# Kernel tuning notes

Hardware: AMD Instinct MI355X
Metric: run time of the kernel (lower is better)

Reference implementation:

```python
import jax, jax.numpy as jnp
import numpy as np

B, S, D = 8, 4096, 256
NUM_WINDOW = 8
WIN = S // NUM_WINDOW          # 512
H = 2                          # num_heads
K = D                          # key_dim = d_model per source
DFF = 1024
LN_EPS = 1e-3                  # keras LayerNormalization default epsilon


def _layer_norm(x, g, b):
    mu = jnp.mean(x, axis=-1, keepdims=True)
    var = jnp.mean(jnp.square(x - mu), axis=-1, keepdims=True)
    return (x - mu) * jax.lax.rsqrt(var + LN_EPS) * g + b


def setup_inputs() -> dict:
    key = jax.random.key(0)
    ks = jax.random.split(key, 12)
    s = 0.02
    inp = {
        "x": jax.random.normal(ks[0], (B, S, D), dtype=jnp.float32),
        # MHA projections (keras MultiHeadAttention layout)
        "Wq": jax.random.normal(ks[1], (D, H, K), dtype=jnp.float32) * s,
        "bq": jnp.zeros((H, K), dtype=jnp.float32),
        "Wk": jax.random.normal(ks[2], (D, H, K), dtype=jnp.float32) * s,
        "bk": jnp.zeros((H, K), dtype=jnp.float32),
        "Wv": jax.random.normal(ks[3], (D, H, K), dtype=jnp.float32) * s,
        "bv": jnp.zeros((H, K), dtype=jnp.float32),
        "Wo": jax.random.normal(ks[4], (H, K, D), dtype=jnp.float32) * s,
        "bo": jnp.zeros((D,), dtype=jnp.float32),
        "ln1_g": jnp.ones((D,), dtype=jnp.float32),
        "ln1_b": jnp.zeros((D,), dtype=jnp.float32),
        # FeedForward
        "W1": jax.random.normal(ks[5], (D, DFF), dtype=jnp.float32) * s,
        "b1": jnp.zeros((DFF,), dtype=jnp.float32),
        "W2": jax.random.normal(ks[6], (DFF, D), dtype=jnp.float32) * s,
        "b2": jnp.zeros((D,), dtype=jnp.float32),
        "ln2_g": jnp.ones((D,), dtype=jnp.float32),
        "ln2_b": jnp.zeros((D,), dtype=jnp.float32),
    }
    return inp


def reference(x, Wq, bq, Wk, bk, Wv, bv, Wo, bo, ln1_g, ln1_b,
              W1, b1, W2, b2, ln2_g, ln2_b):
    # --- Localized self-attention: block-diagonal over NUM_WINDOW windows ---
    xw = x.reshape(B, NUM_WINDOW, WIN, D)               # [b, w, s, d]
    q = jnp.einsum('bwsd,dhk->bwshk', xw, Wq) + bq      # [b, w, s, h, k]
    k = jnp.einsum('bwsd,dhk->bwshk', xw, Wk) + bk
    v = jnp.einsum('bwsd,dhk->bwshk', xw, Wv) + bv
    scores = jnp.einsum('bwshk,bwthk->bwhst', q, k) / jnp.sqrt(
        jnp.asarray(K, dtype=x.dtype))                  # [b, w, h, s, t]
    attn = jax.nn.softmax(scores, axis=-1)
    ctx = jnp.einsum('bwhst,bwthk->bwshk', attn, v)     # [b, w, s, h, k]
    attn_out = jnp.einsum('bwshk,hkd->bwsd', ctx, Wo) + bo
    attn_out = attn_out.reshape(B, S, D)                # concat over windows
    x = _layer_norm(x + attn_out, ln1_g, ln1_b)
    # --- FeedForward (dropout inactive at inference) ---
    h = jax.nn.relu(x @ W1 + b1)
    ff = h @ W2 + b2
    return _layer_norm(x + ff, ln2_g, ln2_b)
```

## Files before the change

### kernel.cpp

```cpp
#include <hip/hip_runtime.h>

typedef unsigned short u16;
typedef short short8 __attribute__((ext_vector_type(8)));
typedef float f32x4 __attribute__((ext_vector_type(4)));

#define AS1C const __attribute__((address_space(1))) void*
#define AS3P __attribute__((address_space(3))) void*

__device__ __forceinline__ u16 f2b(float f) {
  unsigned u = __float_as_uint(f);
  return (u16)((u + 0x7fffu + ((u >> 16) & 1u)) >> 16);
}
__device__ __forceinline__ float b2f(u16 h) {
  return __uint_as_float((unsigned)h << 16);
}

#define BB 8
#define SS 4096
#define DD 256
#define MTOK (BB*SS)

#define OFF_WQKVT  ((size_t)0)
#define OFF_WOT    ((size_t)786432)
#define OFF_W1T    ((size_t)1048576)
#define OFF_W2T    ((size_t)1572864)
#define OFF_BQKV   ((size_t)2097152)
#define OFF_XB     ((size_t)2103296)
#define OFF_QKV    ((size_t)18880512)
#define OFF_YB     ((size_t)52434944)
#define OFF_HB     ((size_t)69212160)
#define OFF_VT     ((size_t)119543808)
#define OFF_CTX    ((size_t)153098240)

__global__ __launch_bounds__(256) void cast_x_kernel(const float* __restrict__ x,
                                                     u16* __restrict__ xb) {
  size_t i = ((size_t)blockIdx.x * 256 + threadIdx.x) * 4;
  float4 v = *(const float4*)(x + i);
  ushort4 o;
  o.x = f2b(v.x); o.y = f2b(v.y); o.z = f2b(v.z); o.w = f2b(v.w);
  *(ushort4*)(xb + i) = o;
}

__global__ __launch_bounds__(256) void prep_w_kernel(
    const float* __restrict__ Wq, const float* __restrict__ Wk, const float* __restrict__ Wv,
    const float* __restrict__ Wo, const float* __restrict__ W1, const float* __restrict__ W2,
    const float* __restrict__ bq, const float* __restrict__ bk, const float* __restrict__ bv,
    u16* __restrict__ wqkvt, u16* __restrict__ wot, u16* __restrict__ w1t,
    u16* __restrict__ w2t, float* __restrict__ bqkv)
{
  for (int i = blockIdx.x * 256 + threadIdx.x; i < 1050112; i += 1024 * 256) {
    if (i < 393216) {
      int n = i >> 8, d = i & 255;
      const float* W = (n < 512) ? Wq : (n < 1024) ? Wk : Wv;
      int nn = n & 511;
      wqkvt[i] = f2b(W[d * 512 + nn]);
    } else if (i < 524288) {
      int j = i - 393216;
      int dout = j >> 9, hk = j & 511;
      wot[j] = f2b(Wo[hk * 256 + dout]);
    } else if (i < 786432) {
      int j = i - 524288;
      int f = j >> 8, d = j & 255;
      w1t[j] = f2b(W1[d * 1024 + f]);
    } else if (i < 1048576) {
      int j = i - 786432;
      int d = j >> 10, f = j & 1023;
      w2t[j] = f2b(W2[f * 256 + d]);
    } else {
      int n = i - 1048576;
      bqkv[n] = (n < 512) ? bq[n] : (n < 1024) ? bk[n - 512] : bv[n - 1024];
    }
  }
}

__global__ __launch_bounds__(256) void gemm_nres(
    const u16* __restrict__ A, const u16* __restrict__ BT,
    const float* __restrict__ bias, u16* __restrict__ C,
    u16* __restrict__ vt, int N, int vbase, int relu)
{
  __shared__ __align__(16) u16 lds[16384];
  const int tid = threadIdx.x, lane = tid & 63, wid = tid >> 6;
  const int ln = lane & 15, quad = lane >> 4;
  const int pn = blockIdx.x >> 5;
  const int mg = blockIdx.x & 31;
  const int wno = (wid >> 1) << 5;
  const int wmo = (wid & 1) << 4;
  const long mbase = (long)mg << 10;
  const int nb = pn << 6;
  const u16* Bp = BT + (size_t)nb * 256;
  const u16* Ap = A + (size_t)mbase * 256;

#pragma unroll
  for (int p = 0; p < 8; p++) {
    const int s = p * 256 + tid;
    const int row = s >> 5, pc = s & 31;
    const int c = pc ^ (row & 31);
    __builtin_amdgcn_global_load_lds(
        (AS1C)(Bp + (size_t)row * 256 + c * 8), (AS3P)(lds + s * 8), 16, 0, 0);
  }
  __syncthreads();
  short8 breg[2][8];
#pragma unroll
  for (int j = 0; j < 2; j++) {
    const int row = wno + j * 16 + ln;
#pragma unroll
    for (int ks = 0; ks < 8; ks++)
      breg[j][ks] = *(const short8*)(lds + row * 256 + (((ks << 2) + quad) ^ (row & 31)) * 8);
  }
  __syncthreads();

#pragma unroll
  for (int p = 0; p < 4; p++) {
    const int s = p * 256 + tid;
    const int row = s >> 5, pc = s & 31;
    const int c = pc ^ (row & 31);
    __builtin_amdgcn_global_load_lds(
        (AS1C)(Ap + (size_t)row * 256 + c * 8), (AS3P)(lds + s * 8), 16, 0, 0);
  }

  for (int it = 0; it < 32; it++) {
    const int cur = it & 1;
    const u16* Ab = lds + cur * 8192;
    __syncthreads();
    if (it + 1 < 32) {
      const u16* An = Ap + (size_t)(it + 1) * 32 * 256;
      u16* Ax = lds + (cur ^ 1) * 8192;
#pragma unroll
      for (int p = 0; p < 4; p++) {
        const int s = p * 256 + tid;
        const int row = s >> 5, pc = s & 31;
        const int c = pc ^ (row & 31);
        __builtin_amdgcn_global_load_lds(
            (AS1C)(An + (size_t)row * 256 + c * 8), (AS3P)(Ax + s * 8), 16, 0, 0);
      }
    }
    f32x4 acc[2];
    acc[0] = (f32x4){0.f, 0.f, 0.f, 0.f};
    acc[1] = (f32x4){0.f, 0.f, 0.f, 0.f};
    const int r0 = wmo + ln;
#pragma unroll
    for (int ks = 0; ks < 8; ks++) {
      const short8 a0 = *(const short8*)(Ab + r0 * 256 + (((ks << 2) + quad) ^ (r0 & 31)) * 8);
      acc[0] = __builtin_amdgcn_mfma_f32_16x16x32_bf16(breg[0][ks], a0, acc[0], 0, 0, 0);
      acc[1] = __builtin_amdgcn_mfma_f32_16x16x32_bf16(breg[1][ks], a0, acc[1], 0, 0, 0);
    }
    const long m = mbase + it * 32 + wmo + ln;
    if (nb < vbase) {
#pragma unroll
      for (int j = 0; j < 2; j++) {
        const int n0 = nb + wno + j * 16 + quad * 4;
        f32x4 v = acc[j];
        const float4 b4 = *(const float4*)(bias + n0);
        v[0] += b4.x; v[1] += b4.y; v[2] += b4.z; v[3] += b4.w;
        if (relu) {
#pragma unroll
          for (int r = 0; r < 4; r++) v[r] = fmaxf(v[r], 0.f);
        }
        ushort4 ob;
        ob.x = f2b(v[0]); ob.y = f2b(v[1]); ob.z = f2b(v[2]); ob.w = f2b(v[3]);
        *(ushort4*)(C + (size_t)m * N + n0) = ob;
      }
    } else {
      const int bw = (int)(m >> 9), t = (int)(m & 511);
#pragma unroll
      for (int j = 0; j < 2; j++) {
        const int n0 = nb + wno + j * 16 + quad * 4;
        const int rel = n0 - vbase;
        const int h = rel >> 8, k0 = rel & 255;
        u16* vp = vt + (size_t)(bw * 2 + h) * 131072 + (size_t)k0 * 512 + t;
        const float4 b4 = *(const float4*)(bias + n0);
        vp[0]    = f2b(acc[j][0] + b4.x);
        vp[512]  = f2b(acc[j][1] + b4.y);
        vp[1024] = f2b(acc[j][2] + b4.z);
        vp[1536] = f2b(acc[j][3] + b4.w);
      }
    }
  }
}

__global__ __launch_bounds__(512) void attn_fused(const u16* __restrict__ qkv,
                                                  const u16* __restrict__ vt,
                                                  u16* __restrict__ ctx)
{
  __shared__ __align__(16) u16 lds[20992];
  const int tid = threadIdx.x, lane = tid & 63, wid = tid >> 6;
  const int ln = lane & 15, quad = lane >> 4;
  const int bat = blockIdx.x & 127, mt = blockIdx.x >> 7;
  const int bw = bat >> 1, h = bat & 1;
  const u16* Qb = qkv + (size_t)bw * 786432 + (size_t)h * 256 + (size_t)(mt * 64) * 1536;
  const u16* Kb = qkv + (size_t)bw * 786432 + 512 + (size_t)h * 256;
  const u16* Vb = vt + (size_t)bat * 131072;
  const int wn = wid * 64;
  float* red1 = (float*)(lds + 18432);
  float* red2 = red1 + 512;

  f32x4 acc[4][4];
#pragma unroll
  for (int i = 0; i < 4; i++)
#pragma unroll
    for (int j = 0; j < 4; j++) acc[i][j] = (f32x4){0.f, 0.f, 0.f, 0.f};

  for (int kt = 0; kt < 256; kt += 32) {
    if (tid < 256) {
      const int row = tid >> 2, c = tid & 3;
      __builtin_amdgcn_global_load_lds(
          (AS1C)(Qb + (size_t)row * 1536 + kt + c * 8), (AS3P)(lds + tid * 8), 16, 0, 0);
    }
#pragma unroll
    for (int p = 0; p < 4; p++) {
      const int s = p * 512 + tid;
      const int row = s >> 2, c = s & 3;
      __builtin_amdgcn_global_load_lds(
          (AS1C)(Kb + (size_t)row * 1536 + kt + c * 8), (AS3P)(lds + 2048 + s * 8), 16, 0, 0);
    }
    __syncthreads();
    short8 a[4], b[4];
#pragma unroll
    for (int i = 0; i < 4; i++) a[i] = *(const short8*)(lds + (i * 16 + ln) * 32 + quad * 8);
#pragma unroll
    for (int j = 0; j < 4; j++) b[j] = *(const short8*)(lds + 2048 + (wn + j * 16 + ln) * 32 + quad * 8);
#pragma unroll
    for (int i = 0; i < 4; i++)
#pragma unroll
      for (int j = 0; j < 4; j++)
        acc[i][j] = __builtin_amdgcn_mfma_f32_16x16x32_bf16(b[j], a[i], acc[i][j], 0, 0, 0);
    __syncthreads();
  }

  float rowmax[4], rowsum[4];
#pragma unroll
  for (int i = 0; i < 4; i++) {
    float m = -1e30f;
#pragma unroll
    for (int j = 0; j < 4; j++)
#pragma unroll
      for (int r = 0; r < 4; r++) m = fmaxf(m, acc[i][j][r]);
    m = fmaxf(m, __shfl_xor(m, 16));
    m = fmaxf(m, __shfl_xor(m, 32));
    if (quad == 0) red1[wid * 64 + i * 16 + ln] = m;
  }
  __syncthreads();
#pragma unroll
  for (int i = 0; i < 4; i++) {
    float m = -1e30f;
#pragma unroll
    for (int w = 0; w < 8; w++) m = fmaxf(m, red1[w * 64 + i * 16 + ln]);
    rowmax[i] = m;
  }
#pragma unroll
  for (int i = 0; i < 4; i++) {
    float s = 0.f;
#pragma unroll
    for (int j = 0; j < 4; j++)
#pragma unroll
      for (int r = 0; r < 4; r++) {
        const float e = __expf((acc[i][j][r] - rowmax[i]) * 0.0625f);
        acc[i][j][r] = e; s += e;
      }
    s += __shfl_xor(s, 16);
    s += __shfl_xor(s, 32);
    if (quad == 0) red2[wid * 64 + i * 16 + ln] = s;
  }
  __syncthreads();
#pragma unroll
  for (int i = 0; i < 4; i++) {
    float s = 0.f;
#pragma unroll
    for (int w = 0; w < 8; w++) s += red2[w * 64 + i * 16 + ln];
    rowsum[i] = 1.f / s;
  }

  u16* Pb = lds;
  u16* Vc = lds + 4608;
  const int wno = wid * 32;
  f32x4 o[4][2];
#pragma unroll
  for (int i = 0; i < 4; i++) {
    o[i][0] = (f32x4){0.f, 0.f, 0.f, 0.f};
    o[i][1] = (f32x4){0.f, 0.f, 0.f, 0.f};
  }

  for (int c = 0; c < 8; c++) {
    __syncthreads();
    if (wid == c) {
#pragma unroll
      for (int i = 0; i < 4; i++)
#pragma unroll
        for (int j = 0; j < 4; j++) {
          ushort4 pb;
          pb.x = f2b(acc[i][j][0] * rowsum[i]);
          pb.y = f2b(acc[i][j][1] * rowsum[i]);
          pb.z = f2b(acc[i][j][2] * rowsum[i]);
          pb.w = f2b(acc[i][j][3] * rowsum[i]);
          *(ushort4*)(Pb + (i * 16 + ln) * 72 + j * 16 + quad * 4) = pb;
        }
    }
#pragma unroll
    for (int p = 0; p < 4; p++) {
      const int s = p * 512 + tid;
      const int row = s >> 3, pc = s & 7;
      const int cc = pc ^ (row & 7);
      __builtin_amdgcn_global_load_lds(
          (AS1C)(Vb + (size_t)row * 512 + c * 64 + cc * 8), (AS3P)(Vc + s * 8), 16, 0, 0);
    }
    __syncthreads();
#pragma unroll
    for (int ks = 0; ks < 2; ks++) {
      short8 ap[4];
#pragma unroll
      for (int i = 0; i < 4; i++)
        ap[i] = *(const short8*)(Pb + (i * 16 + ln) * 72 + ks * 32 + quad * 8);
#pragma unroll
      for (int j = 0; j < 2; j++) {
        const int kV = wno + j * 16 + ln;
        const short8 bv = *(const short8*)(Vc + kV * 64 + (((ks << 2) + quad) ^ (kV & 7)) * 8);
#pragma unroll
        for (int i = 0; i < 4; i++)
          o[i][j] = __builtin_amdgcn_mfma_f32_16x16x32_bf16(bv, ap[i], o[i][j], 0, 0, 0);
      }
    }
  }

  const size_t tokr0 = (size_t)bw * 512 + mt * 64;
#pragma unroll
  for (int i = 0; i < 4; i++) {
    const size_t row = tokr0 + i * 16 + ln;
#pragma unroll
    for (int j = 0; j < 2; j++) {
      const int col = h * 256 + wno + j * 16 + quad * 4;
      ushort4 ob;
      ob.x = f2b(o[i][j][0]); ob.y = f2b(o[i][j][1]);
      ob.z = f2b(o[i][j][2]); ob.w = f2b(o[i][j][3]);
      *(ushort4*)(ctx + row * 512 + col) = ob;
    }
  }
}

__global__ __launch_bounds__(256) void gemm_ln(
    const u16* __restrict__ A, const u16* __restrict__ BT,
    const float* __restrict__ bias, const u16* __restrict__ residb,
    const float* __restrict__ g, const float* __restrict__ beta,
    float* __restrict__ yout, u16* __restrict__ ybout, int K)
{
  __shared__ __align__(16) u16 As[64 * 32];
  __shared__ __align__(16) u16 Bs[256 * 32];
  __shared__ float redS[4][64], redQ[4][64];
  const int tid = threadIdx.x, lane = tid & 63, wid = tid >> 6;
  const int ln = lane & 15, quad = lane >> 4;
  const long bm = (long)blockIdx.x * 64;
  const int wn = wid * 64;
  const u16* Ab = A + (size_t)bm * K;

  f32x4 acc[4][4];
#pragma unroll
  for (int i = 0; i < 4; i++)
#pragma unroll
    for (int j = 0; j < 4; j++) acc[i][j] = (f32x4){0.f, 0.f, 0.f, 0.f};

  for (int kt = 0; kt < K; kt += 32) {
    {
      const int row = tid >> 2, c = tid & 3;
      __builtin_amdgcn_global_load_lds(
          (AS1C)(Ab + (size_t)row * K + kt + c * 8), (AS3P)(As + tid * 8), 16, 0, 0);
    }
#pragma unroll
    for (int p = 0; p < 4; p++) {
      const int s = p * 256 + tid;
      const int row = s >> 2, c = s & 3;
      __builtin_amdgcn_global_load_lds(
          (AS1C)(BT + (size_t)row * K + kt + c * 8), (AS3P)(Bs + s * 8), 16, 0, 0);
    }
    __syncthreads();
    short8 a[4], b[4];
#pragma unroll
    for (int i = 0; i < 4; i++) a[i] = *(const short8*)(As + (i * 16 + ln) * 32 + quad * 8);
#pragma unroll
    for (int j = 0; j < 4; j++) b[j] = *(const short8*)(Bs + (wn + j * 16 + ln) * 32 + quad * 8);
#pragma unroll
    for (int i = 0; i < 4; i++)
#pragma unroll
      for (int j = 0; j < 4; j++)
        acc[i][j] = __builtin_amdgcn_mfma_f32_16x16x32_bf16(b[j], a[i], acc[i][j], 0, 0, 0);
    __syncthreads();
  }

#pragma unroll
  for (int i = 0; i < 4; i++) {
    const long gm = bm + i * 16 + ln;
    float s = 0.f, q = 0.f;
#pragma unroll
    for (int j = 0; j < 4; j++) {
      const int n0 = wn + j * 16 + quad * 4;
      const float4 b4 = *(const float4*)(bias + n0);
      const ushort4 r4 = *(const ushort4*)(residb + (size_t)gm * 256 + n0);
      acc[i][j][0] += b4.x + b2f(r4.x);
      acc[i][j][1] += b4.y + b2f(r4.y);
      acc[i][j][2] += b4.z + b2f(r4.z);
      acc[i][j][3] += b4.w + b2f(r4.w);
#pragma unroll
      for (int r = 0; r < 4; r++) { s += acc[i][j][r]; q += acc[i][j][r] * acc[i][j][r]; }
    }
    s += __shfl_xor(s, 16); s += __shfl_xor(s, 32);
    q += __shfl_xor(q, 16); q += __shfl_xor(q, 32);
    if (quad == 0) { redS[wid][i * 16 + ln] = s; redQ[wid][i * 16 + ln] = q; }
  }
  __syncthreads();
#pragma unroll
  for (int i = 0; i < 4; i++) {
    const long gm = bm + i * 16 + ln;
    float s = 0.f, q = 0.f;
#pragma unroll
    for (int w = 0; w < 4; w++) { s += redS[w][i * 16 + ln]; q += redQ[w][i * 16 + ln]; }
    const float mu = s * (1.f / 256.f);
    const float inv = rsqrtf(q * (1.f / 256.f) - mu * mu + 1e-3f);
#pragma unroll
    for (int j = 0; j < 4; j++) {
      const int n0 = wn + j * 16 + quad * 4;
      const float4 gg = *(const float4*)(g + n0);
      const float4 bb = *(const float4*)(beta + n0);
      float o0 = (acc[i][j][0] - mu) * inv * gg.x + bb.x;
      float o1 = (acc[i][j][1] - mu) * inv * gg.y + bb.y;
      float o2 = (acc[i][j][2] - mu) * inv * gg.z + bb.z;
      float o3 = (acc[i][j][3] - mu) * inv * gg.w + bb.w;
      const size_t off = (size_t)gm * 256 + n0;
      if (yout) {
        float4 o4; o4.x = o0; o4.y = o1; o4.z = o2; o4.w = o3;
        *(float4*)(yout + off) = o4;
      }
      if (ybout) {
        ushort4 ob;
        ob.x = f2b(o0); ob.y = f2b(o1); ob.z = f2b(o2); ob.w = f2b(o3);
        *(ushort4*)(ybout + off) = ob;
      }
    }
  }
}

extern "C" void kernel_launch(void* const* d_in, const int* in_sizes, int n_in,
                              void* d_out, int out_size, void* d_ws, size_t ws_size,
                              hipStream_t stream) {
  (void)in_sizes; (void)n_in; (void)out_size; (void)ws_size;
  const float* x    = (const float*)d_in[0];
  const float* Wq   = (const float*)d_in[1];
  const float* bq   = (const float*)d_in[2];
  const float* Wk   = (const float*)d_in[3];
  const float* bk   = (const float*)d_in[4];
  const float* Wv   = (const float*)d_in[5];
  const float* bv   = (const float*)d_in[6];
  const float* Wo   = (const float*)d_in[7];
  const float* bo   = (const float*)d_in[8];
  const float* ln1g = (const float*)d_in[9];
  const float* ln1b = (const float*)d_in[10];
  const float* W1   = (const float*)d_in[11];
  const float* b1   = (const float*)d_in[12];
  const float* W2   = (const float*)d_in[13];
  const float* b2   = (const float*)d_in[14];
  const float* ln2g = (const float*)d_in[15];
  const float* ln2b = (const float*)d_in[16];
  float* out = (float*)d_out;

  char* ws = (char*)d_ws;
  u16*   WQKVT = (u16*)(ws + OFF_WQKVT);
  u16*   WOT   = (u16*)(ws + OFF_WOT);
  u16*   W1T   = (u16*)(ws + OFF_W1T);
  u16*   W2T   = (u16*)(ws + OFF_W2T);
  float* BQKV  = (float*)(ws + OFF_BQKV);
  u16*   XB    = (u16*)(ws + OFF_XB);
  u16*   QKV   = (u16*)(ws + OFF_QKV);
  u16*   YB    = (u16*)(ws + OFF_YB);
  u16*   HB    = (u16*)(ws + OFF_HB);
  u16*   VT    = (u16*)(ws + OFF_VT);
  u16*   CTX   = (u16*)(ws + OFF_CTX);

  cast_x_kernel<<<8192, 256, 0, stream>>>(x, XB);
  prep_w_kernel<<<1024, 256, 0, stream>>>(Wq, Wk, Wv, Wo, W1, W2, bq, bk, bv,
                                          WQKVT, WOT, W1T, W2T, BQKV);
  gemm_nres<<<768, 256, 0, stream>>>(XB, WQKVT, BQKV, QKV, VT, 1536, 1024, 0);
  attn_fused<<<1024, 512, 0, stream>>>(QKV, VT, CTX);
  gemm_ln<<<512, 256, 0, stream>>>(CTX, WOT, bo, XB, ln1g, ln1b, nullptr, YB, 512);
  gemm_nres<<<512, 256, 0, stream>>>(YB, W1T, b1, HB, nullptr, 1024, 1 << 30, 1);
  gemm_ln<<<512, 256, 0, stream>>>(HB, W2T, b2, YB, ln2g, ln2b, out, nullptr, 1024);
}
```

Before: 370.6 us.

## Double-buffer Q/K and V tiles in attention kernel with MFMA priority boost

```diff
diff --git a/kernel.cpp b/kernel.cpp
--- a/kernel.cpp
+++ b/kernel.cpp
@@ -178,11 +178,11 @@
   }
 }
 
-__global__ __launch_bounds__(512) void attn_fused(const u16* __restrict__ qkv,
-                                                  const u16* __restrict__ vt,
-                                                  u16* __restrict__ ctx)
+__global__ __launch_bounds__(512, 4) void attn_fused(const u16* __restrict__ qkv,
+                                                     const u16* __restrict__ vt,
+                                                     u16* __restrict__ ctx)
 {
-  __shared__ __align__(16) u16 lds[20992];
+  __shared__ __align__(16) u16 lds[38912];
   const int tid = threadIdx.x, lane = tid & 63, wid = tid >> 6;
   const int ln = lane & 15, quad = lane >> 4;
   const int bat = blockIdx.x & 127, mt = blockIdx.x >> 7;
@@ -191,7 +191,7 @@
   const u16* Kb = qkv + (size_t)bw * 786432 + 512 + (size_t)h * 256;
   const u16* Vb = vt + (size_t)bat * 131072;
   const int wn = wid * 64;
-  float* red1 = (float*)(lds + 18432);
+  float* red1 = (float*)(lds + 36864);
   float* red2 = red1 + 512;
 
   f32x4 acc[4][4];
@@ -200,31 +200,53 @@
 #pragma unroll
     for (int j = 0; j < 4; j++) acc[i][j] = (f32x4){0.f, 0.f, 0.f, 0.f};
 
-  for (int kt = 0; kt < 256; kt += 32) {
-    if (tid < 256) {
-      const int row = tid >> 2, c = tid & 3;
-      __builtin_amdgcn_global_load_lds(
-          (AS1C)(Qb + (size_t)row * 1536 + kt + c * 8), (AS3P)(lds + tid * 8), 16, 0, 0);
-    }
-#pragma unroll
-    for (int p = 0; p < 4; p++) {
-      const int s = p * 512 + tid;
-      const int row = s >> 2, c = s & 3;
-      __builtin_amdgcn_global_load_lds(
-          (AS1C)(Kb + (size_t)row * 1536 + kt + c * 8), (AS3P)(lds + 2048 + s * 8), 16, 0, 0);
-    }
+  if (tid < 256) {
+    const int row = tid >> 2, c = tid & 3;
+    __builtin_amdgcn_global_load_lds(
+        (AS1C)(Qb + (size_t)row * 1536 + c * 8), (AS3P)(lds + tid * 8), 16, 0, 0);
+  }
+#pragma unroll
+  for (int p = 0; p < 4; p++) {
+    const int s = p * 512 + tid;
+    const int row = s >> 2, c = s & 3;
+    __builtin_amdgcn_global_load_lds(
+        (AS1C)(Kb + (size_t)row * 1536 + c * 8), (AS3P)(lds + 4096 + s * 8), 16, 0, 0);
+  }
+
+  for (int ki = 0; ki < 8; ki++) {
+    const int cur = ki & 1;
     __syncthreads();
+    if (ki < 7) {
+      const int kt = (ki + 1) * 32, nxt = cur ^ 1;
+      if (tid < 256) {
+        const int row = tid >> 2, c = tid & 3;
+        __builtin_amdgcn_global_load_lds(
+            (AS1C)(Qb + (size_t)row * 1536 + kt + c * 8),
+            (AS3P)(lds + nxt * 2048 + tid * 8), 16, 0, 0);
+      }
+#pragma unroll
+      for (int p = 0; p < 4; p++) {
+        const int s = p * 512 + tid;
+        const int row = s >> 2, c = s & 3;
+        __builtin_amdgcn_global_load_lds(
+            (AS1C)(Kb + (size_t)row * 1536 + kt + c * 8),
+            (AS3P)(lds + 4096 + nxt * 16384 + s * 8), 16, 0, 0);
+      }
+    }
     short8 a[4], b[4];
 #pragma unroll
-    for (int i = 0; i < 4; i++) a[i] = *(const short8*)(lds + (i * 16 + ln) * 32 + quad * 8);
-#pragma unroll
-    for (int j = 0; j < 4; j++) b[j] = *(const short8*)(lds + 2048 + (wn + j * 16 + ln) * 32 + quad * 8);
+    for (int i = 0; i < 4; i++)
+      a[i] = *(const short8*)(lds + cur * 2048 + (i * 16 + ln) * 32 + quad * 8);
+#pragma unroll
+    for (int j = 0; j < 4; j++)
+      b[j] = *(const short8*)(lds + 4096 + cur * 16384 + (wn + j * 16 + ln) * 32 + quad * 8);
+    __builtin_amdgcn_s_setprio(1);
 #pragma unroll
     for (int i = 0; i < 4; i++)
 #pragma unroll
       for (int j = 0; j < 4; j++)
         acc[i][j] = __builtin_amdgcn_mfma_f32_16x16x32_bf16(b[j], a[i], acc[i][j], 0, 0, 0);
-    __syncthreads();
+    __builtin_amdgcn_s_setprio(0);
   }
 
   float rowmax[4], rowsum[4];
@@ -240,6 +262,16 @@
     if (quad == 0) red1[wid * 64 + i * 16 + ln] = m;
   }
   __syncthreads();
+
+#pragma unroll
+  for (int p = 0; p < 4; p++) {
+    const int s = p * 512 + tid;
+    const int row = s >> 3, pc = s & 7;
+    const int cc = pc ^ (row & 7);
+    __builtin_amdgcn_global_load_lds(
+        (AS1C)(Vb + (size_t)row * 512 + cc * 8), (AS3P)(lds + s * 8), 16, 0, 0);
+  }
+
 #pragma unroll
   for (int i = 0; i < 4; i++) {
     float m = -1e30f;
@@ -270,8 +302,18 @@
     rowsum[i] = 1.f / s;
   }
 
-  u16* Pb = lds;
-  u16* Vc = lds + 4608;
+  ushort4 pb[4][4];
+#pragma unroll
+  for (int i = 0; i < 4; i++)
+#pragma unroll
+    for (int j = 0; j < 4; j++) {
+      pb[i][j].x = f2b(acc[i][j][0] * rowsum[i]);
+      pb[i][j].y = f2b(acc[i][j][1] * rowsum[i]);
+      pb[i][j].z = f2b(acc[i][j][2] * rowsum[i]);
+      pb[i][j].w = f2b(acc[i][j][3] * rowsum[i]);
+    }
+
+  u16* Pb = lds + 32768;
   const int wno = wid * 32;
   f32x4 o[4][2];
 #pragma unroll
@@ -286,24 +328,24 @@
 #pragma unroll
       for (int i = 0; i < 4; i++)
 #pragma unroll
-        for (int j = 0; j < 4; j++) {
-          ushort4 pb;
-          pb.x = f2b(acc[i][j][0] * rowsum[i]);
-          pb.y = f2b(acc[i][j][1] * rowsum[i]);
-          pb.z = f2b(acc[i][j][2] * rowsum[i]);
-          pb.w = f2b(acc[i][j][3] * rowsum[i]);
-          *(ushort4*)(Pb + (i * 16 + ln) * 72 + j * 16 + quad * 4) = pb;
-        }
-    }
-#pragma unroll
-    for (int p = 0; p < 4; p++) {
-      const int s = p * 512 + tid;
-      const int row = s >> 3, pc = s & 7;
-      const int cc = pc ^ (row & 7);
-      __builtin_amdgcn_global_load_lds(
-          (AS1C)(Vb + (size_t)row * 512 + c * 64 + cc * 8), (AS3P)(Vc + s * 8), 16, 0, 0);
+        for (int j = 0; j < 4; j++)
+          *(ushort4*)(Pb + (i * 16 + ln) * 72 + j * 16 + quad * 4) = pb[i][j];
     }
     __syncthreads();
+    if (c < 7) {
+      const int nb = (c + 1) & 1;
+#pragma unroll
+      for (int p = 0; p < 4; p++) {
+        const int s = p * 512 + tid;
+        const int row = s >> 3, pc = s & 7;
+        const int cc = pc ^ (row & 7);
+        __builtin_amdgcn_global_load_lds(
+            (AS1C)(Vb + (size_t)row * 512 + (c + 1) * 64 + cc * 8),
+            (AS3P)(lds + nb * 16384 + s * 8), 16, 0, 0);
+      }
+    }
+    const u16* Vc = lds + (c & 1) * 16384;
+    __builtin_amdgcn_s_setprio(1);
 #pragma unroll
     for (int ks = 0; ks < 2; ks++) {
       short8 ap[4];
@@ -319,6 +361,7 @@
           o[i][j] = __builtin_amdgcn_mfma_f32_16x16x32_bf16(bv, ap[i], o[i][j], 0, 0, 0);
       }
     }
+    __builtin_amdgcn_s_setprio(0);
   }
 
   const size_t tokr0 = (size_t)bw * 512 + mt * 64;
```

Result: faster. 338.0 us (-8.8%).

## Load QK operands from global directly, prefetch V in registers, double-buffer GEMM-LN

Applied to the files above, without the earlier changes.

```diff
diff --git a/kernel.cpp b/kernel.cpp
--- a/kernel.cpp
+++ b/kernel.cpp
@@ -178,11 +178,11 @@
   }
 }
 
-__global__ __launch_bounds__(512) void attn_fused(const u16* __restrict__ qkv,
-                                                  const u16* __restrict__ vt,
-                                                  u16* __restrict__ ctx)
+__global__ __launch_bounds__(512, 4) void attn_fused(const u16* __restrict__ qkv,
+                                                     const u16* __restrict__ vt,
+                                                     u16* __restrict__ ctx)
 {
-  __shared__ __align__(16) u16 lds[20992];
+  __shared__ __align__(16) u16 lds[35328];
   const int tid = threadIdx.x, lane = tid & 63, wid = tid >> 6;
   const int ln = lane & 15, quad = lane >> 4;
   const int bat = blockIdx.x & 127, mt = blockIdx.x >> 7;
@@ -191,40 +191,39 @@
   const u16* Kb = qkv + (size_t)bw * 786432 + 512 + (size_t)h * 256;
   const u16* Vb = vt + (size_t)bat * 131072;
   const int wn = wid * 64;
-  float* red1 = (float*)(lds + 18432);
+  const int wno = wid * 32;
+  u16* Pbuf = lds;
+  float* red1 = (float*)(lds + 33280);
   float* red2 = red1 + 512;
 
+  const u16* qp[4];
+  const u16* kp[4];
+#pragma unroll
+  for (int i = 0; i < 4; i++) qp[i] = Qb + (size_t)(i * 16 + ln) * 1536 + quad * 8;
+#pragma unroll
+  for (int j = 0; j < 4; j++) kp[j] = Kb + (size_t)(wn + j * 16 + ln) * 1536 + quad * 8;
+
   f32x4 acc[4][4];
 #pragma unroll
   for (int i = 0; i < 4; i++)
 #pragma unroll
     for (int j = 0; j < 4; j++) acc[i][j] = (f32x4){0.f, 0.f, 0.f, 0.f};
 
-  for (int kt = 0; kt < 256; kt += 32) {
-    if (tid < 256) {
-      const int row = tid >> 2, c = tid & 3;
-      __builtin_amdgcn_global_load_lds(
-          (AS1C)(Qb + (size_t)row * 1536 + kt + c * 8), (AS3P)(lds + tid * 8), 16, 0, 0);
-    }
-#pragma unroll
-    for (int p = 0; p < 4; p++) {
-      const int s = p * 512 + tid;
-      const int row = s >> 2, c = s & 3;
-      __builtin_amdgcn_global_load_lds(
-          (AS1C)(Kb + (size_t)row * 1536 + kt + c * 8), (AS3P)(lds + 2048 + s * 8), 16, 0, 0);
-    }
-    __syncthreads();
+#pragma unroll
+  for (int ki = 0; ki < 8; ki++) {
+    const int kt = ki * 32;
     short8 a[4], b[4];
 #pragma unroll
-    for (int i = 0; i < 4; i++) a[i] = *(const short8*)(lds + (i * 16 + ln) * 32 + quad * 8);
-#pragma unroll
-    for (int j = 0; j < 4; j++) b[j] = *(const short8*)(lds + 2048 + (wn + j * 16 + ln) * 32 + quad * 8);
+    for (int i = 0; i < 4; i++) a[i] = *(const short8*)(qp[i] + kt);
+#pragma unroll
+    for (int j = 0; j < 4; j++) b[j] = *(const short8*)(kp[j] + kt);
+    __builtin_amdgcn_s_setprio(1);
 #pragma unroll
     for (int i = 0; i < 4; i++)
 #pragma unroll
       for (int j = 0; j < 4; j++)
         acc[i][j] = __builtin_amdgcn_mfma_f32_16x16x32_bf16(b[j], a[i], acc[i][j], 0, 0, 0);
-    __syncthreads();
+    __builtin_amdgcn_s_setprio(0);
   }
 
   float rowmax[4], rowsum[4];
@@ -270,9 +269,28 @@
     rowsum[i] = 1.f / s;
   }
 
-  u16* Pb = lds;
-  u16* Vc = lds + 4608;
-  const int wno = wid * 32;
+  short8 vC[2][2], vN[2][2];
+#pragma unroll
+  for (int j = 0; j < 2; j++) {
+    const int kV = wno + j * 16 + ln;
+#pragma unroll
+    for (int ks = 0; ks < 2; ks++)
+      vC[j][ks] = *(const short8*)(Vb + (size_t)kV * 512 + (ks * 4 + quad) * 8);
+  }
+
+#pragma unroll
+  for (int i = 0; i < 4; i++)
+#pragma unroll
+    for (int j = 0; j < 4; j++) {
+      ushort4 pb;
+      pb.x = f2b(acc[i][j][0] * rowsum[i]);
+      pb.y = f2b(acc[i][j][1] * rowsum[i]);
+      pb.z = f2b(acc[i][j][2] * rowsum[i]);
+      pb.w = f2b(acc[i][j][3] * rowsum[i]);
+      *(ushort4*)(Pbuf + (i * 16 + ln) * 520 + wn + j * 16 + quad * 4) = pb;
+    }
+  __syncthreads();
+
   f32x4 o[4][2];
 #pragma unroll
   for (int i = 0; i < 4; i++) {
@@ -280,45 +298,35 @@
     o[i][1] = (f32x4){0.f, 0.f, 0.f, 0.f};
   }
 
+#pragma unroll
   for (int c = 0; c < 8; c++) {
-    __syncthreads();
-    if (wid == c) {
-#pragma unroll
-      for (int i = 0; i < 4; i++)
-#pragma unroll
-        for (int j = 0; j < 4; j++) {
-          ushort4 pb;
-          pb.x = f2b(acc[i][j][0] * rowsum[i]);
-          pb.y = f2b(acc[i][j][1] * rowsum[i]);
-          pb.z = f2b(acc[i][j][2] * rowsum[i]);
-          pb.w = f2b(acc[i][j][3] * rowsum[i]);
-          *(ushort4*)(Pb + (i * 16 + ln) * 72 + j * 16 + quad * 4) = pb;
-        }
-    }
-#pragma unroll
-    for (int p = 0; p < 4; p++) {
-      const int s = p * 512 + tid;
-      const int row = s >> 3, pc = s & 7;
-      const int cc = pc ^ (row & 7);
-      __builtin_amdgcn_global_load_lds(
-          (AS1C)(Vb + (size_t)row * 512 + c * 64 + cc * 8), (AS3P)(Vc + s * 8), 16, 0, 0);
-    }
-    __syncthreads();
+    if (c < 7) {
+#pragma unroll
+      for (int j = 0; j < 2; j++) {
+        const int kV = wno + j * 16 + ln;
+#pragma unroll
+        for (int ks = 0; ks < 2; ks++)
+          vN[j][ks] = *(const short8*)(Vb + (size_t)kV * 512 + (c + 1) * 64 + (ks * 4 + quad) * 8);
+      }
+    }
+    __builtin_amdgcn_s_setprio(1);
 #pragma unroll
     for (int ks = 0; ks < 2; ks++) {
       short8 ap[4];
 #pragma unroll
       for (int i = 0; i < 4; i++)
-        ap[i] = *(const short8*)(Pb + (i * 16 + ln) * 72 + ks * 32 + quad * 8);
-#pragma unroll
-      for (int j = 0; j < 2; j++) {
-        const int kV = wno + j * 16 + ln;
-        const short8 bv = *(const short8*)(Vc + kV * 64 + (((ks << 2) + quad) ^ (kV & 7)) * 8);
+        ap[i] = *(const short8*)(Pbuf + (i * 16 + ln) * 520 + c * 64 + ks * 32 + quad * 8);
+#pragma unroll
+      for (int j = 0; j < 2; j++)
 #pragma unroll
         for (int i = 0; i < 4; i++)
-          o[i][j] = __builtin_amdgcn_mfma_f32_16x16x32_bf16(bv, ap[i], o[i][j], 0, 0, 0);
-      }
-    }
+          o[i][j] = __builtin_amdgcn_mfma_f32_16x16x32_bf16(vC[j][ks], ap[i], o[i][j], 0, 0, 0);
+    }
+    __builtin_amdgcn_s_setprio(0);
+#pragma unroll
+    for (int j = 0; j < 2; j++)
+#pragma unroll
+      for (int ks = 0; ks < 2; ks++) vC[j][ks] = vN[j][ks];
   }
 
   const size_t tokr0 = (size_t)bw * 512 + mt * 64;
@@ -342,14 +350,15 @@
     const float* __restrict__ g, const float* __restrict__ beta,
     float* __restrict__ yout, u16* __restrict__ ybout, int K)
 {
-  __shared__ __align__(16) u16 As[64 * 32];
-  __shared__ __align__(16) u16 Bs[256 * 32];
+  __shared__ __align__(16) u16 As[2][2048];
+  __shared__ __align__(16) u16 Bs[2][8192];
   __shared__ float redS[4][64], redQ[4][64];
   const int tid = threadIdx.x, lane = tid & 63, wid = tid >> 6;
   const int ln = lane & 15, quad = lane >> 4;
   const long bm = (long)blockIdx.x * 64;
   const int wn = wid * 64;
   const u16* Ab = A + (size_t)bm * K;
+  const int nk = K >> 5;
 
   f32x4 acc[4][4];
 #pragma unroll
@@ -357,31 +366,47 @@
 #pragma unroll
     for (int j = 0; j < 4; j++) acc[i][j] = (f32x4){0.f, 0.f, 0.f, 0.f};
 
-  for (int kt = 0; kt < K; kt += 32) {
-    {
+  {
+    const int row = tid >> 2, c = tid & 3;
+    __builtin_amdgcn_global_load_lds(
+        (AS1C)(Ab + (size_t)row * K + c * 8), (AS3P)(&As[0][0] + tid * 8), 16, 0, 0);
+#pragma unroll
+    for (int p = 0; p < 4; p++) {
+      const int s = p * 256 + tid;
+      const int br = s >> 2, bc = s & 3;
+      __builtin_amdgcn_global_load_lds(
+          (AS1C)(BT + (size_t)br * K + bc * 8), (AS3P)(&Bs[0][0] + s * 8), 16, 0, 0);
+    }
+  }
+
+  for (int kti = 0; kti < nk; kti++) {
+    const int cur = kti & 1;
+    __syncthreads();
+    if (kti + 1 < nk) {
+      const int kt = (kti + 1) * 32, nxt = cur ^ 1;
       const int row = tid >> 2, c = tid & 3;
       __builtin_amdgcn_global_load_lds(
-          (AS1C)(Ab + (size_t)row * K + kt + c * 8), (AS3P)(As + tid * 8), 16, 0, 0);
-    }
-#pragma unroll
-    for (int p = 0; p < 4; p++) {
-      const int s = p * 256 + tid;
-      const int row = s >> 2, c = s & 3;
-      __builtin_amdgcn_global_load_lds(
-          (AS1C)(BT + (size_t)row * K + kt + c * 8), (AS3P)(Bs + s * 8), 16, 0, 0);
-    }
-    __syncthreads();
+          (AS1C)(Ab + (size_t)row * K + kt + c * 8), (AS3P)(&As[nxt][0] + tid * 8), 16, 0, 0);
+#pragma unroll
+      for (int p = 0; p < 4; p++) {
+        const int s = p * 256 + tid;
+        const int br = s >> 2, bc = s & 3;
+        __builtin_amdgcn_global_load_lds(
+            (AS1C)(BT + (size_t)br * K + kt + bc * 8), (AS3P)(&Bs[nxt][0] + s * 8), 16, 0, 0);
+      }
+    }
     short8 a[4], b[4];
 #pragma unroll
-    for (int i = 0; i < 4; i++) a[i] = *(const short8*)(As + (i * 16 + ln) * 32 + quad * 8);
-#pragma unroll
-    for (int j = 0; j < 4; j++) b[j] = *(const short8*)(Bs + (wn + j * 16 + ln) * 32 + quad * 8);
+    for (int i = 0; i < 4; i++) a[i] = *(const short8*)(&As[cur][0] + (i * 16 + ln) * 32 + quad * 8);
+#pragma unroll
+    for (int j = 0; j < 4; j++) b[j] = *(const short8*)(&Bs[cur][0] + (wn + j * 16 + ln) * 32 + quad * 8);
+    __builtin_amdgcn_s_setprio(1);
 #pragma unroll
     for (int i = 0; i < 4; i++)
 #pragma unroll
       for (int j = 0; j < 4; j++)
         acc[i][j] = __builtin_amdgcn_mfma_f32_16x16x32_bf16(b[j], a[i], acc[i][j], 0, 0, 0);
-    __syncthreads();
+    __builtin_amdgcn_s_setprio(0);
   }
 
 #pragma unroll
```

New measurement: 367.9 us. No clear change (-0.7%).
